# Kernel tuning notes

Measured on AMD Instinct MI355X. Metric: run time of the kernel, lower is better.

Reference implementation:

```python
import jax, jax.numpy as jnp
import numpy as np

N, E, F = 50000, 800000, 256
EPS = 1e-5


def _agg(h, src, dst, n):
    # gather src node features and sum into dst nodes (DGL copy_src + sum reduce)
    return jax.ops.segment_sum(h[src], dst, num_segments=n)


def _gcn_layer(h, src, dst, W, b):
    n = h.shape[0]
    h = _agg(h, src, dst, n)
    h = _agg(h, src, dst, n)  # update_all is called twice per layer
    return h @ W.T + b


def _batchnorm(h, gamma, beta):
    mean = jnp.mean(h, axis=0)
    var = jnp.mean(jnp.square(h - mean), axis=0)  # biased var, training mode
    return (h - mean) * jax.lax.rsqrt(var + EPS) * gamma + beta


def _branch(feature, src, dst, W1, b1, W2, b2, W3, b3, gamma, beta):
    h = _gcn_layer(feature, src, dst, W1, b1)
    h = _batchnorm(h, gamma, beta)
    h = _gcn_layer(h, src, dst, W2, b2)
    h = _gcn_layer(h, src, dst, W3, b3)
    return h


def setup_inputs() -> dict:
    key = jax.random.key(0)
    ks = jax.random.split(key, 12)
    s = 1.0 / np.sqrt(F)
    return {
        "feature": jax.random.normal(ks[0], (N, F), dtype=jnp.float32),
        "src1": jax.random.randint(ks[1], (E,), 0, N, dtype=jnp.int32),
        "dst1": jax.random.randint(ks[2], (E,), 0, N, dtype=jnp.int32),
        "src2": jax.random.randint(ks[3], (E,), 0, N, dtype=jnp.int32),
        "dst2": jax.random.randint(ks[4], (E,), 0, N, dtype=jnp.int32),
        "W1": jax.random.uniform(ks[5], (F, F), jnp.float32, -s, s),
        "b1": jax.random.uniform(ks[6], (F,), jnp.float32, -s, s),
        "W2": jax.random.uniform(ks[7], (F, F), jnp.float32, -s, s),
        "b2": jax.random.uniform(ks[8], (F,), jnp.float32, -s, s),
        "W3": jax.random.uniform(ks[9], (F, F), jnp.float32, -s, s),
        "b3": jax.random.uniform(ks[10], (F,), jnp.float32, -s, s),
        "gamma": jnp.ones((F,), jnp.float32),
        "beta": jnp.zeros((F,), jnp.float32),
    }


def reference(feature, src1, dst1, src2, dst2, W1, b1, W2, b2, W3, b3, gamma, beta):
    h1 = _branch(feature, src1, dst1, W1, b1, W2, b2, W3, b3, gamma, beta)
    h2 = _branch(feature, src2, dst2, W1, b1, W2, b2, W3, b3, gamma, beta)
    return h1.T @ h2  # [F, F]
```

## Files before the change

### kernel.cpp

```cpp
#include <hip/hip_runtime.h>
#include <hip/hip_fp16.h>

#define FDIM 256
#define GRAM_KS 192


typedef _Float16 f16x8 __attribute__((ext_vector_type(8)));
typedef float f32x4 __attribute__((ext_vector_type(4)));

union H8 { uint2 u2[2]; f16x8 v; };

__device__ __forceinline__ f16x8 ldfrag(const __half* ldsT, int m, int g) {
  H8 h;
  h.u2[0] = *(const uint2*)(ldsT + m * 36 + g * 4);
  h.u2[1] = *(const uint2*)(ldsT + m * 36 + 16 + g * 4);
  return h.v;
}

__device__ __forceinline__ void h8acc(uint4 u, float* a) {
  float2 t;
  t = __half22float2(*(__half2*)&u.x); a[0] += t.x; a[1] += t.y;
  t = __half22float2(*(__half2*)&u.y); a[2] += t.x; a[3] += t.y;
  t = __half22float2(*(__half2*)&u.z); a[4] += t.x; a[5] += t.y;
  t = __half22float2(*(__half2*)&u.w); a[6] += t.x; a[7] += t.y;
}

__global__ void k_hist(const int* __restrict__ dst, int* __restrict__ deg, int E) {
  int e = blockIdx.x * 256 + threadIdx.x;
  if (e < E) atomicAdd(&deg[dst[e]], 1);
}

__global__ __launch_bounds__(256) void k_blksum(const int* __restrict__ deg,
    int* __restrict__ blksum, int n) {
  int b = blockIdx.x, tid = threadIdx.x;
  int base = b * 1024 + tid * 4;
  int s = 0;
#pragma unroll
  for (int k = 0; k < 4; ++k) if (base + k < n) s += deg[base + k];
  for (int off = 32; off; off >>= 1) s += __shfl_down(s, off);
  __shared__ int ws4[4];
  if ((tid & 63) == 0) ws4[tid >> 6] = s;
  __syncthreads();
  if (tid == 0) blksum[b] = ws4[0] + ws4[1] + ws4[2] + ws4[3];
}

__global__ void k_blkscan(const int* __restrict__ blksum, int* __restrict__ blkoff, int nblk) {
  int lane = threadIdx.x;
  int carry = 0;
  for (int base = 0; base < nblk; base += 64) {
    int v = (base + lane < nblk) ? blksum[base + lane] : 0;
    int x = v;
    for (int off = 1; off < 64; off <<= 1) { int y = __shfl_up(x, off); if (lane >= off) x += y; }
    if (base + lane < nblk) blkoff[base + lane] = carry + x - v;
    carry += __shfl(x, 63);
  }
}

__global__ __launch_bounds__(256) void k_scan_blk(const int* __restrict__ deg,
    const int* __restrict__ blkoff, int* __restrict__ rowptr, int* __restrict__ cursor, int n) {
  int b = blockIdx.x, tid = threadIdx.x;
  int base = b * 1024 + tid * 4;
  int v[4];
#pragma unroll
  for (int k = 0; k < 4; ++k) v[k] = (base + k < n) ? deg[base + k] : 0;
  int s = v[0] + v[1] + v[2] + v[3];
  int lane = tid & 63, w = tid >> 6;
  int x = s;
  for (int off = 1; off < 64; off <<= 1) { int y = __shfl_up(x, off); if (lane >= off) x += y; }
  __shared__ int wsum[4];
  if (lane == 63) wsum[w] = x;
  __syncthreads();
  int wadd = 0;
  for (int i = 0; i < w; ++i) wadd += wsum[i];
  int run = blkoff[b] + wadd + x - s;
#pragma unroll
  for (int k = 0; k < 4; ++k) {
    if (base + k < n) { rowptr[base + k] = run; cursor[base + k] = run; }
    run += v[k];
  }
  if (n >= base && n <= base + 4) rowptr[n] = run;
}

__global__ void k_scatter(const int* __restrict__ src, const int* __restrict__ dst,
    int* __restrict__ cursor, int* __restrict__ esrc, int E) {
  int e = blockIdx.x * 256 + threadIdx.x;
  if (e < E) {
    int p = atomicAdd(&cursor[dst[e]], 1);
    esrc[p] = src[e];
  }
}

__global__ __launch_bounds__(256) void k_tr2(const float* __restrict__ W2,
    const float* __restrict__ W3, float* __restrict__ W2T, float* __restrict__ W3T) {
  __shared__ float tile[64][65];
  const float* src = blockIdx.z ? W3 : W2;
  float* dst = blockIdx.z ? W3T : W2T;
  int i0 = blockIdx.x * 64, j0 = blockIdx.y * 64;
  int tx = threadIdx.x & 63, ty = threadIdx.x >> 6;
#pragma unroll
  for (int m = 0; m < 16; ++m) {
    int r = ty * 16 + m;
    tile[r][tx] = src[(size_t)(i0 + r) * 256 + j0 + tx];
  }
  __syncthreads();
#pragma unroll
  for (int m = 0; m < 16; ++m) {
    int r = ty * 16 + m;
    dst[(size_t)(j0 + r) * 256 + i0 + tx] = tile[tx][r];
  }
}

__global__ __launch_bounds__(256) void k_f2h(const float* __restrict__ F,
    __half* __restrict__ H, int n4) {
  int i = blockIdx.x * 256 + threadIdx.x;
  if (i >= n4) return;
  float4 v = ((const float4*)F)[i];
  __half2 a = __floats2half2_rn(v.x, v.y);
  __half2 b = __floats2half2_rn(v.z, v.w);
  uint2 u; u.x = *(unsigned int*)&a; u.y = *(unsigned int*)&b;
  ((uint2*)H)[i] = u;
}

__global__ __launch_bounds__(256) void k_aggh(const __half* __restrict__ h,
    const int* __restrict__ rowptr, const int* __restrict__ esrc,
    __half* __restrict__ out, int n) {
  int wid = ((blockIdx.x * 256) + threadIdx.x) >> 6;
  int lane = threadIdx.x & 63;
  if (wid >= n) return;
  int half = lane >> 5, l5 = lane & 31;
  int beg = rowptr[wid], end = rowptr[wid + 1];
  int m = end - beg;
  const uint4* hv = (const uint4*)h;
  float a0[8] = {}, a1[8] = {}, a2[8] = {}, a3[8] = {};
  int g8 = m >> 3;
  int e = beg + half;
  for (int it = 0; it < g8; ++it, e += 8) {
    int s0 = esrc[e], s1 = esrc[e + 2], s2 = esrc[e + 4], s3 = esrc[e + 6];
    uint4 u0 = hv[(size_t)s0 * 32 + l5];
    uint4 u1 = hv[(size_t)s1 * 32 + l5];
    uint4 u2 = hv[(size_t)s2 * 32 + l5];
    uint4 u3 = hv[(size_t)s3 * 32 + l5];
    h8acc(u0, a0); h8acc(u1, a1); h8acc(u2, a2); h8acc(u3, a3);
  }
  for (; e < end; e += 2) {
    uint4 u = hv[(size_t)esrc[e] * 32 + l5];
    h8acc(u, a0);
  }
  float s[8];
#pragma unroll
  for (int j = 0; j < 8; ++j) {
    s[j] = (a0[j] + a1[j]) + (a2[j] + a3[j]);
    s[j] += __shfl_xor(s[j], 32);
    s[j] *= 0.25f;
  }
  if (half == 0) {
    __half2 h0 = __floats2half2_rn(s[0], s[1]);
    __half2 h1 = __floats2half2_rn(s[2], s[3]);
    __half2 h2 = __floats2half2_rn(s[4], s[5]);
    __half2 h3 = __floats2half2_rn(s[6], s[7]);
    uint4 uo;
    uo.x = *(unsigned int*)&h0; uo.y = *(unsigned int*)&h1;
    uo.z = *(unsigned int*)&h2; uo.w = *(unsigned int*)&h3;
    ((uint4*)out)[(size_t)wid * 32 + l5] = uo;
  }
}

__global__ __launch_bounds__(256) void k_aggv2(const float* __restrict__ in1,
    const float* __restrict__ in2,
    const int* __restrict__ rp1, const int* __restrict__ es1,
    const int* __restrict__ rp2, const int* __restrict__ es2,
    float* __restrict__ out1, float* __restrict__ out2, int n, int useDeg) {
  int t = blockIdx.x * 256 + threadIdx.x;
  int g = t >> 4;
  int sl = t & 15;
  if (g >= 2 * n) return;
  int which = (g >= n) ? 1 : 0;
  int node = which ? g - n : g;
  const int* rp = which ? rp2 : rp1;
  const int* es = which ? es2 : es1;
  const float* in = which ? in2 : in1;
  float* out = which ? out2 : out1;
  int beg = rp[node], end = rp[node + 1];
  float s = 0.f;
  if (useDeg) {
    for (int e = beg + sl; e < end; e += 16) {
      int v = es[e];
      s += (float)(rp[v + 1] - rp[v]);
    }
  } else {
    for (int e = beg + sl; e < end; e += 16) s += in[es[e]];
  }
#pragma unroll
  for (int off = 8; off; off >>= 1) s += __shfl_down(s, off, 16);
  if (sl == 0) out[node] = s;
}

__global__ __launch_bounds__(256) void k_gram_sym(const __half* __restrict__ Xm,
    float* __restrict__ partial, int N, float* __restrict__ mc) {
  __shared__ __half ldsA[128 * 36];
  __shared__ __half ldsB[128 * 36];
  int tid = threadIdx.x;
  int t = blockIdx.x;
  int i0 = (t == 2) ? 128 : 0;
  int j0 = (t == 0) ? 0 : 128;
  bool diag = (t != 1);
  int z = blockIdx.z;
  int chunk = (N + GRAM_KS - 1) / GRAM_KS;
  int rb = z * chunk, re = min(N, rb + chunk);
  int lane = tid & 63, w = tid >> 6;
  int g = lane >> 4;
  int lm = lane & 15;
  int wm = w >> 1, wn = w & 1;
  int sp = tid >> 4;
  int sc = (tid & 15) * 8;
  int cc = tid & 127, hh = tid >> 7;
  float xP = 0.f;
  f32x4 acc[4][4] = {};
  const __half* Bsrc = diag ? ldsA : ldsB;
  for (int rr = rb; rr < re; rr += 32) {
    int r0 = rr + 2 * sp, r1 = r0 + 1;
    uint4 a0 = {0,0,0,0}, a1 = {0,0,0,0}, b0 = {0,0,0,0}, b1 = {0,0,0,0};
    if (r0 < re) a0 = *(const uint4*)(Xm + (size_t)r0 * 256 + i0 + sc);
    if (r1 < re) a1 = *(const uint4*)(Xm + (size_t)r1 * 256 + i0 + sc);
    if (!diag) {
      if (r0 < re) b0 = *(const uint4*)(Xm + (size_t)r0 * 256 + j0 + sc);
      if (r1 < re) b1 = *(const uint4*)(Xm + (size_t)r1 * 256 + j0 + sc);
    }
    __syncthreads();
    {
      const unsigned short* pa0 = (const unsigned short*)&a0;
      const unsigned short* pa1 = (const unsigned short*)&a1;
      const unsigned short* pb0 = (const unsigned short*)&b0;
      const unsigned short* pb1 = (const unsigned short*)&b1;
#pragma unroll
      for (int j = 0; j < 8; ++j) {
        *(unsigned int*)(ldsA + (sc + j) * 36 + 2 * sp) =
            (unsigned int)pa0[j] | ((unsigned int)pa1[j] << 16);
        if (!diag)
          *(unsigned int*)(ldsB + (sc + j) * 36 + 2 * sp) =
              (unsigned int)pb0[j] | ((unsigned int)pb1[j] << 16);
      }
    }
    __syncthreads();
    if (diag && mc) {
      const __half* p = ldsA + cc * 36 + hh * 16;
#pragma unroll
      for (int k = 0; k < 16; ++k) xP += __half2float(p[k]);
    }
    f16x8 af[4];
#pragma unroll
    for (int fm = 0; fm < 4; ++fm) af[fm] = ldfrag(ldsA, wm * 64 + fm * 16 + lm, g);
#pragma unroll
    for (int fn = 0; fn < 4; ++fn) {
      f16x8 bf = ldfrag(Bsrc, wn * 64 + fn * 16 + lm, g);
#pragma unroll
      for (int fm = 0; fm < 4; ++fm)
        acc[fm][fn] = __builtin_amdgcn_mfma_f32_16x16x32_f16(af[fm], bf, acc[fm][fn], 0, 0, 0);
    }
  }
  float* pout = partial + (size_t)z * 65536;
#pragma unroll
  for (int fm = 0; fm < 4; ++fm) {
#pragma unroll
    for (int reg = 0; reg < 4; ++reg) {
      int row = i0 + wm * 64 + fm * 16 + g * 4 + reg;
#pragma unroll
      for (int fn = 0; fn < 4; ++fn) {
        int col = j0 + wn * 64 + fn * 16 + lm;
        pout[(size_t)row * 256 + col] = acc[fm][fn][reg];
      }
    }
  }
  if (diag && mc) {
    __syncthreads();
    float* fs = (float*)ldsA;
    fs[hh * 128 + cc] = xP;
    __syncthreads();
    if (tid < 128) atomicAdd(&mc[i0 + tid], (fs[tid] + fs[128 + tid]) * 16.0f);
  }
}

__global__ void k_gram_reduce_sym(const float* __restrict__ partial, float* __restrict__ C) {
  int idx = blockIdx.x * 256 + threadIdx.x;
  int i = idx >> 8, j = idx & 255;
  int sidx = (i >= 128 && j < 128) ? (j * 256 + i) : idx;
  float s = 0.f;
  for (int z = 0; z < GRAM_KS; ++z) s += partial[(size_t)z * 65536 + sidx];
  C[idx] = s * 256.0f;
}

__global__ __launch_bounds__(256) void k_gram(const __half* __restrict__ Xm,
    const __half* __restrict__ Ym, float* __restrict__ partial, int N,
    const float* __restrict__ wxA, const float* __restrict__ wxB, float* __restrict__ outX,
    const float* __restrict__ wyA, const float* __restrict__ wyB, float* __restrict__ outY) {
  __shared__ __half ldsA[128 * 36];
  __shared__ __half ldsB[128 * 36];
  __shared__ float wls[4][32];
  int tid = threadIdx.x;
  int i0 = blockIdx.x * 128, j0 = blockIdx.y * 128;
  int z = blockIdx.z;
  int chunk = (N + GRAM_KS - 1) / GRAM_KS;
  int rb = z * chunk, re = min(N, rb + chunk);
  int lane = tid & 63, w = tid >> 6;
  int g = lane >> 4;
  int lm = lane & 15;
  int wm = w >> 1, wn = w & 1;
  int sp = tid >> 4;
  int sc = (tid & 15) * 8;
  bool doX = (outX != nullptr) && (blockIdx.y == 0);
  bool doY = (outY != nullptr) && (blockIdx.x == 0);
  int cc = tid & 127, hh = tid >> 7;
  float xA = 0, xB = 0, xP = 0, yA = 0, yB = 0, yP = 0;
  f32x4 acc[4][4] = {};
  for (int rr = rb; rr < re; rr += 32) {
    int r0 = rr + 2 * sp, r1 = r0 + 1;
    uint4 a0 = {0,0,0,0}, a1 = {0,0,0,0}, b0 = {0,0,0,0}, b1 = {0,0,0,0};
    if (r0 < re) {
      a0 = *(const uint4*)(Xm + (size_t)r0 * 256 + i0 + sc);
      b0 = *(const uint4*)(Ym + (size_t)r0 * 256 + j0 + sc);
    }
    if (r1 < re) {
      a1 = *(const uint4*)(Xm + (size_t)r1 * 256 + i0 + sc);
      b1 = *(const uint4*)(Ym + (size_t)r1 * 256 + j0 + sc);
    }
    __syncthreads();
    {
      const unsigned short* pa0 = (const unsigned short*)&a0;
      const unsigned short* pa1 = (const unsigned short*)&a1;
      const unsigned short* pb0 = (const unsigned short*)&b0;
      const unsigned short* pb1 = (const unsigned short*)&b1;
#pragma unroll
      for (int j = 0; j < 8; ++j) {
        *(unsigned int*)(ldsA + (sc + j) * 36 + 2 * sp) =
            (unsigned int)pa0[j] | ((unsigned int)pa1[j] << 16);
        *(unsigned int*)(ldsB + (sc + j) * 36 + 2 * sp) =
            (unsigned int)pb0[j] | ((unsigned int)pb1[j] << 16);
      }
    }
    if (tid < 128) {
      int grp = tid >> 5, kk = tid & 31, rw = rr + kk;
      const float* wp = (grp == 0) ? wxA : (grp == 1) ? wxB : (grp == 2) ? wyA : wyB;
      wls[grp][kk] = (wp && rw < re) ? wp[rw] : 0.f;
    }
    __syncthreads();
    if (doX) {
      const __half* p = ldsA + cc * 36 + hh * 16;
#pragma unroll
      for (int k = 0; k < 16; ++k) {
        float v = __half2float(p[k]);
        xP += v; xA += v * wls[0][hh * 16 + k]; xB += v * wls[1][hh * 16 + k];
      }
    }
    if (doY) {
      const __half* p = ldsB + cc * 36 + hh * 16;
#pragma unroll
      for (int k = 0; k < 16; ++k) {
        float v = __half2float(p[k]);
        yP += v; yA += v * wls[2][hh * 16 + k]; yB += v * wls[3][hh * 16 + k];
      }
    }
    f16x8 af[4];
#pragma unroll
    for (int fm = 0; fm < 4; ++fm) af[fm] = ldfrag(ldsA, wm * 64 + fm * 16 + lm, g);
#pragma unroll
    for (int fn = 0; fn < 4; ++fn) {
      f16x8 bf = ldfrag(ldsB, wn * 64 + fn * 16 + lm, g);
#pragma unroll
      for (int fm = 0; fm < 4; ++fm)
        acc[fm][fn] = __builtin_amdgcn_mfma_f32_16x16x32_f16(af[fm], bf, acc[fm][fn], 0, 0, 0);
    }
  }
  float* pout = partial + (size_t)z * 65536;
#pragma unroll
  for (int fm = 0; fm < 4; ++fm) {
#pragma unroll
    for (int reg = 0; reg < 4; ++reg) {
      int row = i0 + wm * 64 + fm * 16 + g * 4 + reg;
#pragma unroll
      for (int fn = 0; fn < 4; ++fn) {
        int col = j0 + wn * 64 + fn * 16 + lm;
        pout[(size_t)row * 256 + col] = acc[fm][fn][reg];
      }
    }
  }
  const float S6 = 4096.0f;
  float* fs = (float*)ldsA;
  if (doX) {
    __syncthreads();
    fs[hh * 128 + cc] = xA;
    __syncthreads();
    if (tid < 128) atomicAdd(&outX[i0 + tid], (fs[tid] + fs[128 + tid]) * S6);
    __syncthreads();
    fs[hh * 128 + cc] = xB;
    __syncthreads();
    if (tid < 128) atomicAdd(&outX[256 + i0 + tid], (fs[tid] + fs[128 + tid]) * S6);
    __syncthreads();
    fs[hh * 128 + cc] = xP;
    __syncthreads();
    if (tid < 128) atomicAdd(&outX[512 + i0 + tid], (fs[tid] + fs[128 + tid]) * S6);
  }
  if (doY) {
    __syncthreads();
    fs[hh * 128 + cc] = yA;
    __syncthreads();
    if (tid < 128) atomicAdd(&outY[j0 + tid], (fs[tid] + fs[128 + tid]) * S6);
    __syncthreads();
    fs[hh * 128 + cc] = yB;
    __syncthreads();
    if (tid < 128) atomicAdd(&outY[256 + j0 + tid], (fs[tid] + fs[128 + tid]) * S6);
    __syncthreads();
    fs[hh * 128 + cc] = yP;
    __syncthreads();
    if (tid < 128) atomicAdd(&outY[512 + j0 + tid], (fs[tid] + fs[128 + tid]) * S6);
  }
}

__global__ void k_gram_reduce(const float* __restrict__ partial, float* __restrict__ C) {
  int idx = blockIdx.x * 256 + threadIdx.x;
  float s = 0.f;
  for (int z = 0; z < GRAM_KS; ++z) s += partial[(size_t)z * 65536 + idx];
  C[idx] = s * 16777216.0f;
}

__global__ __launch_bounds__(256) void k_dots(const float* __restrict__ d1,
    const float* __restrict__ e1, const float* __restrict__ d2,
    const float* __restrict__ e2, float* scal, int n) {
  float s[8] = {};
  for (int i = blockIdx.x * 256 + threadIdx.x; i < n; i += gridDim.x * 256) {
    float a = d1[i], b = e1[i], c = d2[i], d = e2[i];
    s[0] += b * d; s[1] += b * c; s[2] += b; s[3] += a * d;
    s[4] += a * c; s[5] += a; s[6] += d; s[7] += c;
  }
  __shared__ float red[4][8];
  int lane = threadIdx.x & 63, w = threadIdx.x >> 6;
#pragma unroll
  for (int j = 0; j < 8; ++j)
    for (int off = 32; off; off >>= 1) s[j] += __shfl_down(s[j], off);
  if (lane == 0)
#pragma unroll
    for (int j = 0; j < 8; ++j) red[w][j] = s[j];
  __syncthreads();
  if (threadIdx.x < 8) {
    int j = threadIdx.x;
    atomicAdd(&scal[j], red[0][j] + red[1][j] + red[2][j] + red[3][j]);
  }
}

__global__ __launch_bounds__(256) void k_quad(const float* __restrict__ C,
    const float* __restrict__ W1, const float* __restrict__ m_raw,
    float* __restrict__ t, float* __restrict__ mv) {
  __shared__ float w[256];
  __shared__ float r1[256], r2[256];
  int j = blockIdx.x, tid = threadIdx.x;
  w[tid] = W1[j * 256 + tid];
  __syncthreads();
  float v = 0.f;
  for (int k = 0; k < 256; ++k) v += w[k] * C[k * 256 + tid];
  r1[tid] = v * w[tid];
  r2[tid] = w[tid] * m_raw[tid];
  __syncthreads();
  for (int off = 128; off; off >>= 1) {
    if (tid < off) { r1[tid] += r1[tid + off]; r2[tid] += r2[tid + off]; }
    __syncthreads();
  }
  if (tid == 0) { t[j] = r1[0]; mv[j] = r2[0]; }
}

__global__ __launch_bounds__(256) void k_bncoef(const float* __restrict__ t,
    const float* __restrict__ mv, const float* __restrict__ b1,
    const float* __restrict__ gamma, const float* __restrict__ beta,
    const float* __restrict__ W2T, const float* __restrict__ W3T,
    const float* __restrict__ b2, float* Dv, float* xv, float* yv, int n) {
  __shared__ float c[256], u[256];
  int j = threadIdx.x;
  float invn = 1.f / (float)n;
  float mean = mv[j] * invn + b1[j];
  float E2 = t[j] * invn + 2.f * b1[j] * mv[j] * invn + b1[j] * b1[j];
  float var = E2 - mean * mean;
  float D = gamma[j] * rsqrtf(var + 1e-5f);
  Dv[j] = D;
  c[j] = D * (b1[j] - mean) + beta[j];
  __syncthreads();
  float uu = 0.f;
  for (int k = 0; k < 256; ++k) uu += W2T[k * 256 + j] * c[k];
  u[j] = uu;
  __syncthreads();
  float xx = 0.f, yy = 0.f;
  for (int k = 0; k < 256; ++k) {
    xx += W3T[k * 256 + j] * u[k];
    yy += W3T[k * 256 + j] * b2[k];
  }
  xv[j] = xx;
  yv[j] = yy;
}

__global__ __launch_bounds__(256) void k_mm_small(float* __restrict__ Cm,
    const float* __restrict__ A, const float* __restrict__ B,
    const float* __restrict__ s, int transA) {
  __shared__ float a[256];
  int i = blockIdx.x, j = threadIdx.x;
  float av = transA ? A[j * 256 + i] : A[i * 256 + j];
  a[j] = s ? av * s[j] : av;
  __syncthreads();
  float acc = 0.f;
  for (int k = 0; k < 256; ++k) acc += a[k] * B[k * 256 + j];
  Cm[i * 256 + j] = acc;
}

__global__ __launch_bounds__(256) void k_mv6(const float* __restrict__ R1,
    const float* __restrict__ R2, const float* __restrict__ pX,
    const float* __restrict__ qY, float* __restrict__ vout) {
  __shared__ float w[256];
  int b = blockIdx.x, j = threadIdx.x;
  const float* M = (b < 3) ? R1 : R2;
  const float* wv = (b < 3) ? (pX + b * 256) : (qY + (b - 3) * 256);
  w[j] = wv[j];
  __syncthreads();
  float s = 0.f;
  for (int k = 0; k < 256; ++k) s += M[k * 256 + j] * w[k];
  vout[b * 256 + j] = s;
}

__global__ __launch_bounds__(256) void k_mm_final(float* __restrict__ out,
    const float* __restrict__ R1, const float* __restrict__ T1,
    const float* __restrict__ vout,
    const float* __restrict__ x1, const float* __restrict__ x2,
    const float* __restrict__ yv, const float* __restrict__ b3,
    const float* __restrict__ scal, float fN) {
  __shared__ float a[256];
  int i = blockIdx.x, j = threadIdx.x;
  a[j] = R1[j * 256 + i];
  __syncthreads();
  float acc = 0.f;
  for (int k = 0; k < 256; ++k) acc += a[k] * T1[k * 256 + j];
  float s1 = scal[0] * x2[j] + scal[1] * yv[j] + scal[2] * b3[j];
  float s2 = scal[3] * x2[j] + scal[4] * yv[j] + scal[5] * b3[j];
  float s3 = scal[6] * x2[j] + scal[7] * yv[j] + fN * b3[j];
  acc += vout[i] * x2[j] + vout[256 + i] * yv[j] + vout[512 + i] * b3[j];
  acc += x1[i] * (vout[768 + j] + s1) + yv[i] * (vout[1024 + j] + s2)
       + b3[i] * (vout[1280 + j] + s3);
  out[i * 256 + j] = acc;
}

extern "C" void kernel_launch(void* const* d_in, const int* in_sizes, int n_in,
                              void* d_out, int out_size, void* d_ws, size_t ws_size,
                              hipStream_t stream) {
  const float* feature = (const float*)d_in[0];
  const int* src1 = (const int*)d_in[1];
  const int* dst1 = (const int*)d_in[2];
  const int* src2 = (const int*)d_in[3];
  const int* dst2 = (const int*)d_in[4];
  const float* W1 = (const float*)d_in[5];
  const float* b1 = (const float*)d_in[6];
  const float* W2 = (const float*)d_in[7];
  const float* b2 = (const float*)d_in[8];
  const float* W3 = (const float*)d_in[9];
  const float* b3 = (const float*)d_in[10];
  const float* gamma = (const float*)d_in[11];
  const float* beta = (const float*)d_in[12];
  const int N = in_sizes[0] / FDIM;
  const int E = in_sizes[1];
  float* out = (float*)d_out;

  size_t NF = (size_t)N * FDIM;
  __half* FH = (__half*)d_ws;
  __half* Xh = FH + NF;
  __half* Yh = Xh + NF;
  __half* G2A = Yh + NF;
  float* partial = (float*)(G2A + NF);
  int* rowptr1 = (int*)(partial + (size_t)GRAM_KS * 65536);
  int* rowptr2 = rowptr1 + (N + 1);
  int* cursor = rowptr2 + (N + 1);
  int* esrc1 = cursor + N;
  int* esrc2 = esrc1 + E;
  float* vtmp1 = (float*)(esrc2 + E);
  float* vtmp2 = vtmp1 + N;
  float* d1 = vtmp2 + N; float* e1 = d1 + N; float* d2 = e1 + N; float* e2 = d2 + N;
  float* C = e2 + N;
  float* mcA = C + 65536;
  float* mcB = mcA + 256;
  float* pX = mcB + 256;
  float* qY = pX + 768;
  float* scal = qY + 768;
  float* tq = scal + 16; float* mv = tq + 256;
  float* Dv = mv + 256; float* x1 = Dv + 256; float* x2 = x1 + 256; float* yv = x2 + 256;
  float* Q = yv + 256; float* R1 = Q + 65536; float* R2 = R1 + 65536;
  float* Z = R2 + 65536; float* T1 = Z + 65536;
  float* W2T = T1 + 65536; float* W3T = W2T + 65536;
  float* vout = W3T + 65536;
  int* blksum = (int*)(vout + 1536);
  int* blkoff = blksum + 1024;

  const int eb = (E + 255) / 256;
  const int aggb = (N + 3) / 4;
  const int avb2 = (2 * N * 16 + 255) / 256;
  const int nblk = (N + 1023) / 1024;

  auto build = [&](const int* s_, const int* d_, int* rp, int* es) {
    hipMemsetAsync(cursor, 0, (size_t)N * sizeof(int), stream);
    k_hist<<<eb, 256, 0, stream>>>(d_, cursor, E);
    k_blksum<<<nblk, 256, 0, stream>>>(cursor, blksum, N);
    k_blkscan<<<1, 64, 0, stream>>>(blksum, blkoff, nblk);
    k_scan_blk<<<nblk, 256, 0, stream>>>(cursor, blkoff, rp, cursor, N);
    k_scatter<<<eb, 256, 0, stream>>>(s_, d_, cursor, es, E);
  };

  k_tr2<<<dim3(4, 4, 2), 256, 0, stream>>>(W2, W3, W2T, W3T);
  k_f2h<<<(int)((NF / 4 + 255) / 256), 256, 0, stream>>>(feature, FH, (int)(NF / 4));
  build(src1, dst1, rowptr1, esrc1);
  build(src2, dst2, rowptr2, esrc2);
  hipMemsetAsync(mcA, 0, (256 * 2 + 768 * 2 + 16) * sizeof(float), stream);

  k_aggv2<<<avb2, 256, 0, stream>>>(nullptr, nullptr, rowptr1, esrc1, rowptr2, esrc2,
                                    d1, d2, N, 1);
  k_aggv2<<<avb2, 256, 0, stream>>>(d1, d2, rowptr1, esrc1, rowptr2, esrc2,
                                    vtmp1, vtmp2, N, 0);
  k_aggv2<<<avb2, 256, 0, stream>>>(vtmp1, vtmp2, rowptr1, esrc1, rowptr2, esrc2,
                                    e1, e2, N, 0);
  k_dots<<<64, 256, 0, stream>>>(d1, e1, d2, e2, scal, N);

  auto do_branch = [&](const int* rp, const int* es, __half* G2dst,
                       float* mc, float* xvec, float* Rdst) {
    k_aggh<<<aggb, 256, 0, stream>>>(FH, rp, es, Xh, N);
    k_aggh<<<aggb, 256, 0, stream>>>(Xh, rp, es, Yh, N);
    k_gram_sym<<<dim3(3, 1, GRAM_KS), 256, 0, stream>>>(Yh, partial, N, mc);
    k_gram_reduce_sym<<<256, 256, 0, stream>>>(partial, C);
    k_quad<<<256, 256, 0, stream>>>(C, W1, mc, tq, mv);
    k_bncoef<<<1, 256, 0, stream>>>(tq, mv, b1, gamma, beta, W2T, W3T, b2, Dv, xvec, yv, N);
    k_mm_small<<<256, 256, 0, stream>>>(Q, W1, W2T, Dv, 1);
    k_mm_small<<<256, 256, 0, stream>>>(Rdst, Q, W3T, nullptr, 0);
    k_aggh<<<aggb, 256, 0, stream>>>(Yh, rp, es, Xh, N);
    k_aggh<<<aggb, 256, 0, stream>>>(Xh, rp, es, Yh, N);
    k_aggh<<<aggb, 256, 0, stream>>>(Yh, rp, es, Xh, N);
    k_aggh<<<aggb, 256, 0, stream>>>(Xh, rp, es, G2dst, N);
  };

  do_branch(rowptr1, esrc1, G2A, mcA, x1, R1);
  do_branch(rowptr2, esrc2, Yh, mcB, x2, R2);

  k_gram<<<dim3(2, 2, GRAM_KS), 256, 0, stream>>>(G2A, Yh, partial, N,
      e2, d2, pX, e1, d1, qY);
  k_gram_reduce<<<256, 256, 0, stream>>>(partial, Z);

  k_mm_small<<<256, 256, 0, stream>>>(T1, Z, R2, nullptr, 0);
  k_mv6<<<6, 256, 0, stream>>>(R1, R2, pX, qY, vout);
  k_mm_final<<<256, 256, 0, stream>>>(out, R1, T1, vout, x1, x2, yv, b3, scal, (float)N);
}
```

Before: 1.295 ms.

## Two-pass bucketed CSR scatter, deeper gather unroll, smaller Gram K-split

The one-pass atomic CSR scatter is replaced by two passes. The first partitions edges into 64 coarse destination buckets, staging them in LDS and writing each bucket contiguously. The second does a per-bucket scatter so the atomics and writes stay within a localized node range. The aggregation loop is unrolled to 8 gathers in flight per iteration, and the Gram K-split constant is halved. The extra pass and extra pairs traffic could offset the locality gain, and k_scat2 with only 64 blocks may underfill the GPU.

```diff
diff --git a/kernel.cpp b/kernel.cpp
--- a/kernel.cpp
+++ b/kernel.cpp
@@ -2,7 +2,8 @@
 #include <hip/hip_fp16.h>
 
 #define FDIM 256
-#define GRAM_KS 192
+#define GRAM_KS 96
+#define NB 64
 
 
 typedef _Float16 f16x8 __attribute__((ext_vector_type(8)));
@@ -81,12 +82,73 @@
   if (n >= base && n <= base + 4) rowptr[n] = run;
 }
 
-__global__ void k_scatter(const int* __restrict__ src, const int* __restrict__ dst,
-    int* __restrict__ cursor, int* __restrict__ esrc, int E) {
-  int e = blockIdx.x * 256 + threadIdx.x;
-  if (e < E) {
-    int p = atomicAdd(&cursor[dst[e]], 1);
-    esrc[p] = src[e];
+__global__ void k_binit(const int* __restrict__ rowptr, int* __restrict__ gcur,
+    int N, int bshift) {
+  int b = threadIdx.x;
+  if (b < NB) {
+    int idx = b << bshift;
+    if (idx > N) idx = N;
+    gcur[b] = rowptr[idx];
+  }
+}
+
+__global__ __launch_bounds__(256) void k_part(const int* __restrict__ src,
+    const int* __restrict__ dst, int* __restrict__ gcur, int2* __restrict__ pairs,
+    int E, int bshift) {
+  __shared__ int cnt[NB];
+  __shared__ int lbase[NB];
+  __shared__ int gbase[NB];
+  __shared__ int tot;
+  __shared__ int2 stg[4096];
+  int tid = threadIdx.x;
+  int e0 = blockIdx.x * 4096;
+  if (tid < NB) cnt[tid] = 0;
+  __syncthreads();
+  int es[16], ed[16], lp[16];
+#pragma unroll
+  for (int k = 0; k < 16; ++k) {
+    int e = e0 + k * 256 + tid;
+    lp[k] = -1;
+    if (e < E) {
+      es[k] = src[e]; ed[k] = dst[e];
+      lp[k] = atomicAdd(&cnt[ed[k] >> bshift], 1);
+    }
+  }
+  __syncthreads();
+  if (tid < NB) {
+    int v = cnt[tid];
+    int x = v;
+    for (int off = 1; off < NB; off <<= 1) { int y = __shfl_up(x, off); if (tid >= off) x += y; }
+    lbase[tid] = x - v;
+    gbase[tid] = atomicAdd(&gcur[tid], v);
+    if (tid == NB - 1) tot = x;
+  }
+  __syncthreads();
+#pragma unroll
+  for (int k = 0; k < 16; ++k) {
+    if (lp[k] >= 0) stg[lbase[ed[k] >> bshift] + lp[k]] = make_int2(es[k], ed[k]);
+  }
+  __syncthreads();
+  int T = tot;
+  for (int i = tid; i < T; i += 256) {
+    int2 p = stg[i];
+    int b = p.y >> bshift;
+    pairs[gbase[b] + (i - lbase[b])] = p;
+  }
+}
+
+__global__ __launch_bounds__(512) void k_scat2(const int2* __restrict__ pairs,
+    const int* __restrict__ rowptr, int* __restrict__ cursor, int* __restrict__ esrc,
+    int N, int bshift) {
+  int b = blockIdx.x;
+  int i0 = b << bshift, i1 = (b + 1) << bshift;
+  if (i0 > N) i0 = N;
+  if (i1 > N) i1 = N;
+  int lo = rowptr[i0], hi = rowptr[i1];
+  for (int i = lo + threadIdx.x; i < hi; i += 512) {
+    int2 p = pairs[i];
+    int pos = atomicAdd(&cursor[p.y], 1);
+    esrc[pos] = p.x;
   }
 }
 
@@ -129,12 +191,24 @@
   if (wid >= n) return;
   int half = lane >> 5, l5 = lane & 31;
   int beg = rowptr[wid], end = rowptr[wid + 1];
-  int m = end - beg;
   const uint4* hv = (const uint4*)h;
   float a0[8] = {}, a1[8] = {}, a2[8] = {}, a3[8] = {};
-  int g8 = m >> 3;
   int e = beg + half;
-  for (int it = 0; it < g8; ++it, e += 8) {
+  for (; e + 14 < end; e += 16) {
+    int s0 = esrc[e], s1 = esrc[e + 2], s2 = esrc[e + 4], s3 = esrc[e + 6];
+    int s4 = esrc[e + 8], s5 = esrc[e + 10], s6 = esrc[e + 12], s7 = esrc[e + 14];
+    uint4 u0 = hv[(size_t)s0 * 32 + l5];
+    uint4 u1 = hv[(size_t)s1 * 32 + l5];
+    uint4 u2 = hv[(size_t)s2 * 32 + l5];
+    uint4 u3 = hv[(size_t)s3 * 32 + l5];
+    uint4 u4 = hv[(size_t)s4 * 32 + l5];
+    uint4 u5 = hv[(size_t)s5 * 32 + l5];
+    uint4 u6 = hv[(size_t)s6 * 32 + l5];
+    uint4 u7 = hv[(size_t)s7 * 32 + l5];
+    h8acc(u0, a0); h8acc(u1, a1); h8acc(u2, a2); h8acc(u3, a3);
+    h8acc(u4, a0); h8acc(u5, a1); h8acc(u6, a2); h8acc(u7, a3);
+  }
+  for (; e + 6 < end; e += 8) {
     int s0 = esrc[e], s1 = esrc[e + 2], s2 = esrc[e + 4], s3 = esrc[e + 6];
     uint4 u0 = hv[(size_t)s0 * 32 + l5];
     uint4 u1 = hv[(size_t)s1 * 32 + l5];
@@ -590,11 +664,17 @@
   float* vout = W3T + 65536;
   int* blksum = (int*)(vout + 1536);
   int* blkoff = blksum + 1024;
+  int* gcur = blkoff + 1024;
+  int2* pairs = (int2*)partial;
 
   const int eb = (E + 255) / 256;
   const int aggb = (N + 3) / 4;
   const int avb2 = (2 * N * 16 + 255) / 256;
   const int nblk = (N + 1023) / 1024;
+  int bshift = 0;
+  while (((N - 1) >> bshift) >= NB) ++bshift;
+  const int nbk = ((N - 1) >> bshift) + 1;
+  const int pb = (E + 4095) / 4096;
 
   auto build = [&](const int* s_, const int* d_, int* rp, int* es) {
     hipMemsetAsync(cursor, 0, (size_t)N * sizeof(int), stream);
@@ -602,7 +682,9 @@
     k_blksum<<<nblk, 256, 0, stream>>>(cursor, blksum, N);
     k_blkscan<<<1, 64, 0, stream>>>(blksum, blkoff, nblk);
     k_scan_blk<<<nblk, 256, 0, stream>>>(cursor, blkoff, rp, cursor, N);
-    k_scatter<<<eb, 256, 0, stream>>>(s_, d_, cursor, es, E);
+    k_binit<<<1, 64, 0, stream>>>(rp, gcur, N, bshift);
+    k_part<<<pb, 256, 0, stream>>>(s_, d_, gcur, pairs, E, bshift);
+    k_scat2<<<nbk, 512, 0, stream>>>(pairs, rp, cursor, es, N, bshift);
   };
 
   k_tr2<<<dim3(4, 4, 2), 256, 0, stream>>>(W2, W3, W2T, W3T);
```

After: 1.365 ms. 5.4% more time.
